# Performance work log

Hardware: AMD Instinct MI355X
Metric: run time of the kernel (lower is better)

Reference implementation:

```python
import jax, jax.numpy as jnp
import numpy as np

EMBED_DIM = 1024
NUM_HEADS = 16
HEAD_DIM = EMBED_DIM // NUM_HEADS


def setup_inputs() -> dict:
    key = jax.random.key(0)
    k_x, k_qkv, k_proj, k_pb = jax.random.split(key, 4)
    B, N = 8, 1024
    s = 1.0 / np.sqrt(EMBED_DIM)
    return {
        "x": jax.random.normal(k_x, (B, N, EMBED_DIM), dtype=jnp.float32),
        # qkv: Linear(embed_dim -> 3*all_head_dim), bias=False
        "w_qkv": jax.random.uniform(k_qkv, (EMBED_DIM, 3 * EMBED_DIM), dtype=jnp.float32, minval=-s, maxval=s),
        # proj: Linear(all_head_dim -> embed_dim), with bias
        "w_proj": jax.random.uniform(k_proj, (EMBED_DIM, EMBED_DIM), dtype=jnp.float32, minval=-s, maxval=s),
        "b_proj": jax.random.uniform(k_pb, (EMBED_DIM,), dtype=jnp.float32, minval=-s, maxval=s),
    }


def reference(x, w_qkv, w_proj, b_proj):
    B, N, _ = x.shape
    scale = HEAD_DIM ** -0.5
    qkv = jnp.einsum("bnd,de->bne", x, w_qkv)  # [B, N, 3*D]
    q, k, v = jnp.split(qkv, 3, axis=-1)
    # reshape to heads: [B, H, N, hd]
    def heads(t):
        return t.reshape(B, N, NUM_HEADS, HEAD_DIM).transpose(0, 2, 1, 3)
    q, k, v = heads(q), heads(k), heads(v)
    attn = jnp.einsum("bhqd,bhkd->bhqk", q, k) * scale
    attn = jax.nn.softmax(attn, axis=-1)
    out = jnp.einsum("bhqk,bhkd->bhqd", attn, v)
    out = out.transpose(0, 2, 1, 3).reshape(B, N, NUM_HEADS * HEAD_DIM)
    return jnp.einsum("bnd,de->bne", out, w_proj) + b_proj
```

## Files before the change

kernel.cpp:

```cpp
#include <hip/hip_runtime.h>
#include <hip/hip_bf16.h>
#include <stdint.h>

typedef __hip_bfloat16 bf16;
typedef __attribute__((ext_vector_type(8))) __bf16 bf16x8;
typedef __attribute__((ext_vector_type(4))) float f32x4;

__device__ __forceinline__ bf16x8 load8bf(const bf16* p) {
    return __builtin_bit_cast(bf16x8, *(const int4*)p);
}

__device__ __forceinline__ void async16(const bf16* g, bf16* l) {
    __builtin_amdgcn_global_load_lds((const __attribute__((address_space(1))) void*)g,
                                     (__attribute__((address_space(3))) void*)l, 16, 0, 0);
}

__global__ __launch_bounds__(256) void cast_x_kernel(const float* __restrict__ in,
                                                     bf16* __restrict__ out, int n4) {
    int i = blockIdx.x * 256 + threadIdx.x;
    if (i >= n4) return;
    float4 v = ((const float4*)in)[i];
    ushort4 o;
    o.x = __builtin_bit_cast(unsigned short, __float2bfloat16(v.x));
    o.y = __builtin_bit_cast(unsigned short, __float2bfloat16(v.y));
    o.z = __builtin_bit_cast(unsigned short, __float2bfloat16(v.z));
    o.w = __builtin_bit_cast(unsigned short, __float2bfloat16(v.w));
    ((ushort4*)out)[i] = o;
}

__global__ __launch_bounds__(256) void transpose_cast(const float* __restrict__ in,
                                                      bf16* __restrict__ out, int R, int C) {
    __shared__ float t[32][33];
    int c0 = blockIdx.x * 32, r0 = blockIdx.y * 32;
    int tx = threadIdx.x, ty = threadIdx.y;
#pragma unroll
    for (int j = 0; j < 32; j += 8)
        t[ty + j][tx] = in[(size_t)(r0 + ty + j) * C + c0 + tx];
    __syncthreads();
#pragma unroll
    for (int j = 0; j < 32; j += 8)
        out[(size_t)(c0 + ty + j) * R + r0 + tx] = __float2bfloat16(t[tx][ty + j]);
}

template <int MODE>
__global__ __launch_bounds__(256) void gemm_bt(
    const bf16* __restrict__ A, const bf16* __restrict__ Bt,
    int M, int N, int K,
    bf16* __restrict__ qo, bf16* __restrict__ ko, bf16* __restrict__ vto,
    float* __restrict__ out, const float* __restrict__ bias) {
    __shared__ __align__(16) bf16 Al0[128 * 64];
    __shared__ __align__(16) bf16 Bl0[128 * 64];
    __shared__ __align__(16) bf16 Al1[128 * 64];
    __shared__ __align__(16) bf16 Bl1[128 * 64];
    const int tid = threadIdx.x;
    const int l = tid & 63, wid = tid >> 6;
    const int lo = l & 15, hi = l >> 4;
    const int wm = wid >> 1, wn = wid & 1;
    const int m0 = blockIdx.x * 128, n0 = blockIdx.y * 128;
    const int sr = tid >> 3;
    const int cl = (tid & 7) * 8;
    const int csw = ((tid & 7) ^ (sr & 7)) * 8;

    f32x4 acc[4][4];
#pragma unroll
    for (int i = 0; i < 4; ++i)
#pragma unroll
        for (int j = 0; j < 4; ++j) acc[i][j] = f32x4{0.f, 0.f, 0.f, 0.f};

#define STAGE_A(DST, KT)                                                              \
    _Pragma("unroll") for (int s_ = 0; s_ < 4; ++s_) {                                \
        int r_ = s_ * 32 + sr;                                                        \
        async16(A + (size_t)(m0 + r_) * K + (KT) * 64 + csw, DST + r_ * 64 + cl);     \
    }
#define STAGE_B(DST, KT)                                                              \
    _Pragma("unroll") for (int s_ = 0; s_ < 4; ++s_) {                                \
        int r_ = s_ * 32 + sr;                                                        \
        async16(Bt + (size_t)(n0 + r_) * K + (KT) * 64 + csw, DST + r_ * 64 + cl);    \
    }
#define KBODY(AL, BL, ANXT, BNXT, KT, STG)                                            \
    {                                                                                 \
        __syncthreads();        \
        if (STG) { STAGE_A(ANXT, (KT) + 1); }                                         \
        __builtin_amdgcn_sched_barrier(0);                                            \
        bf16x8 af[4][2], bfv0[2][2];                                                  \
        _Pragma("unroll") for (int mt = 0; mt < 4; ++mt) {                            \
            int ar = wm * 64 + mt * 16 + lo;                                          \
            _Pragma("unroll") for (int ks = 0; ks < 2; ++ks)                          \
                af[mt][ks] = load8bf(AL + ar * 64 + ((ks * 32 + hi * 8) ^ ((ar & 7) * 8))); \
        }                                                                             \
        _Pragma("unroll") for (int nt = 0; nt < 2; ++nt) {                            \
            int br = wn * 64 + nt * 16 + lo;                                          \
            _Pragma("unroll") for (int ks = 0; ks < 2; ++ks)                          \
                bfv0[nt][ks] = load8bf(BL + br * 64 + ((ks * 32 + hi * 8) ^ ((br & 7) * 8))); \
        }                                                                             \
        _Pragma("unroll") for (int mt = 0; mt < 4; ++mt)                              \
            _Pragma("unroll") for (int nt = 0; nt < 2; ++nt)                          \
                _Pragma("unroll") for (int ks = 0; ks < 2; ++ks)                      \
                    acc[mt][nt] = __builtin_amdgcn_mfma_f32_16x16x32_bf16(            \
                        af[mt][ks], bfv0[nt][ks], acc[mt][nt], 0, 0, 0);              \
        if (STG) { STAGE_B(BNXT, (KT) + 1); }                                         \
        __builtin_amdgcn_sched_barrier(0);                                            \
        bf16x8 bfv1[2][2];                                                            \
        _Pragma("unroll") for (int nt = 0; nt < 2; ++nt) {                            \
            int br = wn * 64 + (nt + 2) * 16 + lo;                                    \
            _Pragma("unroll") for (int ks = 0; ks < 2; ++ks)                          \
                bfv1[nt][ks] = load8bf(BL + br * 64 + ((ks * 32 + hi * 8) ^ ((br & 7) * 8))); \
        }                                                                             \
        _Pragma("unroll") for (int mt = 0; mt < 4; ++mt)                              \
            _Pragma("unroll") for (int nt = 0; nt < 2; ++nt)                          \
                _Pragma("unroll") for (int ks = 0; ks < 2; ++ks)                      \
                    acc[mt][nt + 2] = __builtin_amdgcn_mfma_f32_16x16x32_bf16(        \
                        af[mt][ks], bfv1[nt][ks], acc[mt][nt + 2], 0, 0, 0);          \
    }

    const int nkt = K / 64;
    STAGE_A(Al0, 0)
    STAGE_B(Bl0, 0)
    for (int kt = 0; kt < nkt; kt += 2) {
        KBODY(Al0, Bl0, Al1, Bl1, kt, true)
        KBODY(Al1, Bl1, Al0, Bl0, kt + 1, (kt + 2 < nkt))
    }
#undef KBODY
#undef STAGE_B
#undef STAGE_A

#pragma unroll
    for (int mt = 0; mt < 4; ++mt)
#pragma unroll
        for (int nt = 0; nt < 4; ++nt)
#pragma unroll
            for (int r = 0; r < 4; ++r) {
                int row = m0 + wm * 64 + mt * 16 + hi * 4 + r;
                int col = n0 + wn * 64 + nt * 16 + lo;
                float v = acc[mt][nt][r];
                if (MODE == 0) {
                    if (col < 1024) {
                        qo[(size_t)row * 1024 + col] = __float2bfloat16(v * 0.125f);
                    } else if (col < 2048) {
                        ko[(size_t)row * 1024 + (col - 1024)] = __float2bfloat16(v);
                    } else {
                        int c = col - 2048;
                        vto[((size_t)(row >> 10) * 1024 + c) * 1024 + (row & 1023)] = __float2bfloat16(v);
                    }
                } else {
                    out[(size_t)row * N + col] = v + bias[col];
                }
            }
}

__global__ __launch_bounds__(256, 4) void flash_attn(
    const bf16* __restrict__ q,
    const bf16* __restrict__ kin,
    const bf16* __restrict__ vt,
    bf16* __restrict__ out)
{
    __shared__ __align__(16) bf16 Kl[64 * 72];
    __shared__ __align__(16) bf16 Vl[64 * 72];
    __shared__ __align__(16) bf16 Pl[4 * 32 * 72];
    const int tid = threadIdx.x;
    const int l = tid & 63, w = tid >> 6;
    const int lo = l & 15, hi = l >> 4;
    const int bid = (blockIdx.x & 7) * 128 + (blockIdx.x >> 3);
    const int qt = bid & 7, h = (bid >> 3) & 15, b = bid >> 7;
    const int sr = tid >> 3;
    const int sc = (tid & 7) * 8;

    const bf16* kbase = kin + (size_t)(b * 1024) * 1024 + h * 64;
    const bf16* vbase = vt + (size_t)(b * 1024 + h * 64) * 1024;

    bf16x8 qf[2][2];
#pragma unroll
    for (int mt = 0; mt < 2; ++mt)
#pragma unroll
        for (int ks = 0; ks < 2; ++ks) {
            int tok = qt * 128 + w * 32 + mt * 16 + lo;
            qf[mt][ks] = load8bf(q + (size_t)(b * 1024 + tok) * 1024 + h * 64 + ks * 32 + hi * 8);
        }

    float lsum[2][4];
    f32x4 oacc[2][4];
#pragma unroll
    for (int mt = 0; mt < 2; ++mt)
#pragma unroll
        for (int r = 0; r < 4; ++r) lsum[mt][r] = 0.f;
#pragma unroll
    for (int mt = 0; mt < 2; ++mt)
#pragma unroll
        for (int nt = 0; nt < 4; ++nt) oacc[mt][nt] = f32x4{0.f, 0.f, 0.f, 0.f};

    int4 kreg[2], vreg[2];
#pragma unroll
    for (int it = 0; it < 2; ++it) {
        int r = it * 32 + sr;
        kreg[it] = *(const int4*)(kbase + (size_t)r * 1024 + sc);
        vreg[it] = *(const int4*)(vbase + (size_t)r * 1024 + sc);
    }
#pragma unroll
    for (int it = 0; it < 2; ++it) {
        int r = it * 32 + sr;
        *(int4*)(Kl + r * 72 + sc) = kreg[it];
        *(int4*)(Vl + r * 72 + sc) = vreg[it];
    }
    __syncthreads();

    for (int kt = 0; kt < 16; ++kt) {
        if (kt < 15) {
#pragma unroll
            for (int it = 0; it < 2; ++it) {
                int r = it * 32 + sr;
                kreg[it] = *(const int4*)(kbase + (size_t)((kt + 1) * 64 + r) * 1024 + sc);
                vreg[it] = *(const int4*)(vbase + (size_t)r * 1024 + (kt + 1) * 64 + sc);
            }
        }

        f32x4 s[2][4];
#pragma unroll
        for (int mt = 0; mt < 2; ++mt)
#pragma unroll
            for (int nt = 0; nt < 4; ++nt) s[mt][nt] = f32x4{0.f, 0.f, 0.f, 0.f};
#pragma unroll
        for (int ks = 0; ks < 2; ++ks) {
            bf16x8 kf[4];
#pragma unroll
            for (int nt = 0; nt < 4; ++nt)
                kf[nt] = load8bf(Kl + (nt * 16 + lo) * 72 + ks * 32 + hi * 8);
#pragma unroll
            for (int mt = 0; mt < 2; ++mt)
#pragma unroll
                for (int nt = 0; nt < 4; ++nt)
                    s[mt][nt] = __builtin_amdgcn_mfma_f32_16x16x32_bf16(qf[mt][ks], kf[nt], s[mt][nt], 0, 0, 0);
        }

#pragma unroll
        for (int mt = 0; mt < 2; ++mt)
#pragma unroll
            for (int nt = 0; nt < 4; ++nt)
#pragma unroll
                for (int r = 0; r < 4; ++r) {
                    float p = __expf(s[mt][nt][r]);
                    lsum[mt][r] += p;
                    Pl[(w * 32 + mt * 16 + hi * 4 + r) * 72 + nt * 16 + lo] = __float2bfloat16(p);
                }

#pragma unroll
        for (int ks = 0; ks < 2; ++ks) {
            bf16x8 vf[4], pf[2];
#pragma unroll
            for (int nt = 0; nt < 4; ++nt)
                vf[nt] = load8bf(Vl + (nt * 16 + lo) * 72 + ks * 32 + hi * 8);
#pragma unroll
            for (int mt = 0; mt < 2; ++mt)
                pf[mt] = load8bf(Pl + (w * 32 + mt * 16 + lo) * 72 + ks * 32 + hi * 8);
#pragma unroll
            for (int mt = 0; mt < 2; ++mt)
#pragma unroll
                for (int nt = 0; nt < 4; ++nt)
                    oacc[mt][nt] = __builtin_amdgcn_mfma_f32_16x16x32_bf16(pf[mt], vf[nt], oacc[mt][nt], 0, 0, 0);
        }
        __syncthreads();

        if (kt < 15) {
#pragma unroll
            for (int it = 0; it < 2; ++it) {
                int r = it * 32 + sr;
                *(int4*)(Kl + r * 72 + sc) = kreg[it];
                *(int4*)(Vl + r * 72 + sc) = vreg[it];
            }
            __syncthreads();
        }
    }

#pragma unroll
    for (int mt = 0; mt < 2; ++mt)
#pragma unroll
        for (int r = 0; r < 4; ++r) {
#pragma unroll
            for (int off = 1; off < 16; off <<= 1)
                lsum[mt][r] += __shfl_xor(lsum[mt][r], off);
        }

#pragma unroll
    for (int mt = 0; mt < 2; ++mt)
#pragma unroll
        for (int nt = 0; nt < 4; ++nt)
#pragma unroll
            for (int r = 0; r < 4; ++r) {
                int tok = qt * 128 + w * 32 + mt * 16 + hi * 4 + r;
                int d = nt * 16 + lo;
                out[(size_t)(b * 1024 + tok) * 1024 + h * 64 + d] =
                    __float2bfloat16(oacc[mt][nt][r] / lsum[mt][r]);
            }
}

extern "C" void kernel_launch(void* const* d_in, const int* in_sizes, int n_in,
                              void* d_out, int out_size, void* d_ws, size_t ws_size,
                              hipStream_t stream) {
    const float* x      = (const float*)d_in[0];
    const float* w_qkv  = (const float*)d_in[1];
    const float* w_proj = (const float*)d_in[2];
    const float* b_proj = (const float*)d_in[3];
    float* out = (float*)d_out;

    char* ws = (char*)d_ws;
    bf16* xb     = (bf16*)(ws);
    bf16* wqkvT  = (bf16*)(ws + (16ull << 20));
    bf16* wprojT = (bf16*)(ws + (22ull << 20));
    bf16* qb     = (bf16*)(ws + (24ull << 20));
    bf16* kb     = (bf16*)(ws + (40ull << 20));
    bf16* vtb    = (bf16*)(ws + (56ull << 20));
    bf16* attn   = xb;

    cast_x_kernel<<<8192, 256, 0, stream>>>(x, xb, 2 * 1024 * 1024);
    transpose_cast<<<dim3(96, 32), dim3(32, 8), 0, stream>>>(w_qkv, wqkvT, 1024, 3072);
    transpose_cast<<<dim3(32, 32), dim3(32, 8), 0, stream>>>(w_proj, wprojT, 1024, 1024);
    gemm_bt<0><<<dim3(64, 24), 256, 0, stream>>>(xb, wqkvT, 8192, 3072, 1024,
                                                 qb, kb, vtb, nullptr, nullptr);
    flash_attn<<<1024, 256, 0, stream>>>(qb, kb, vtb, attn);
    gemm_bt<1><<<dim3(64, 8), 256, 0, stream>>>(attn, wprojT, 8192, 1024, 1024,
                                                nullptr, nullptr, nullptr, out, b_proj);
}
```

Baseline: 186.6 us.

## Double-buffer K/V tiles with async global-to-LDS loads and XOR swizzle

Replaces the register-staged K/V prefetch in the flash attention kernel with direct global_load_lds async copies into two ping-pong LDS buffers. The loop is unrolled by two so each iteration issues the next tile's copy before computing on the current one, which drops one barrier per tile. The padded 72-wide LDS rows become 64-wide rows with an XOR swizzle to avoid bank conflicts. The extra buffers raise LDS use, so the launch-bounds occupancy hint falls from 4 to 3 blocks, which may reduce latency hiding.

```diff
diff --git a/kernel.cpp b/kernel.cpp
--- a/kernel.cpp
+++ b/kernel.cpp
@@ -148,25 +148,39 @@
             }
 }
 
-__global__ __launch_bounds__(256, 4) void flash_attn(
+__global__ __launch_bounds__(256, 3) void flash_attn(
     const bf16* __restrict__ q,
     const bf16* __restrict__ kin,
     const bf16* __restrict__ vt,
     bf16* __restrict__ out)
 {
-    __shared__ __align__(16) bf16 Kl[64 * 72];
-    __shared__ __align__(16) bf16 Vl[64 * 72];
+    __shared__ __align__(16) bf16 Kl0[64 * 64];
+    __shared__ __align__(16) bf16 Vl0[64 * 64];
+    __shared__ __align__(16) bf16 Kl1[64 * 64];
+    __shared__ __align__(16) bf16 Vl1[64 * 64];
     __shared__ __align__(16) bf16 Pl[4 * 32 * 72];
     const int tid = threadIdx.x;
     const int l = tid & 63, w = tid >> 6;
     const int lo = l & 15, hi = l >> 4;
     const int bid = (blockIdx.x & 7) * 128 + (blockIdx.x >> 3);
     const int qt = bid & 7, h = (bid >> 3) & 15, b = bid >> 7;
-    const int sr = tid >> 3;
-    const int sc = (tid & 7) * 8;
+    const int ts_r = tid >> 3;
+    const int ts_c = tid & 7;
+    const int ts_csw = (ts_c ^ (ts_r & 7)) * 8;
+    const int ts_lds = tid * 8;
 
     const bf16* kbase = kin + (size_t)(b * 1024) * 1024 + h * 64;
     const bf16* vbase = vt + (size_t)(b * 1024 + h * 64) * 1024;
+
+#define STAGE_KV(KD, VD, KT)                                                          \
+    {                                                                                 \
+        async16(kbase + (size_t)((KT) * 64 + ts_r) * 1024 + ts_csw, (KD) + ts_lds);   \
+        async16(kbase + (size_t)((KT) * 64 + 32 + ts_r) * 1024 + ts_csw,              \
+                (KD) + 2048 + ts_lds);                                                \
+        async16(vbase + (size_t)ts_r * 1024 + (KT) * 64 + ts_csw, (VD) + ts_lds);     \
+        async16(vbase + (size_t)(32 + ts_r) * 1024 + (KT) * 64 + ts_csw,              \
+                (VD) + 2048 + ts_lds);                                                \
+    }
 
     bf16x8 qf[2][2];
 #pragma unroll
@@ -188,87 +202,58 @@
 #pragma unroll
         for (int nt = 0; nt < 4; ++nt) oacc[mt][nt] = f32x4{0.f, 0.f, 0.f, 0.f};
 
-    int4 kreg[2], vreg[2];
-#pragma unroll
-    for (int it = 0; it < 2; ++it) {
-        int r = it * 32 + sr;
-        kreg[it] = *(const int4*)(kbase + (size_t)r * 1024 + sc);
-        vreg[it] = *(const int4*)(vbase + (size_t)r * 1024 + sc);
-    }
-#pragma unroll
-    for (int it = 0; it < 2; ++it) {
-        int r = it * 32 + sr;
-        *(int4*)(Kl + r * 72 + sc) = kreg[it];
-        *(int4*)(Vl + r * 72 + sc) = vreg[it];
-    }
+    STAGE_KV(Kl0, Vl0, 0)
     __syncthreads();
 
-    for (int kt = 0; kt < 16; ++kt) {
-        if (kt < 15) {
-#pragma unroll
-            for (int it = 0; it < 2; ++it) {
-                int r = it * 32 + sr;
-                kreg[it] = *(const int4*)(kbase + (size_t)((kt + 1) * 64 + r) * 1024 + sc);
-                vreg[it] = *(const int4*)(vbase + (size_t)r * 1024 + (kt + 1) * 64 + sc);
-            }
-        }
-
-        f32x4 s[2][4];
-#pragma unroll
-        for (int mt = 0; mt < 2; ++mt)
-#pragma unroll
-            for (int nt = 0; nt < 4; ++nt) s[mt][nt] = f32x4{0.f, 0.f, 0.f, 0.f};
-#pragma unroll
-        for (int ks = 0; ks < 2; ++ks) {
-            bf16x8 kf[4];
-#pragma unroll
-            for (int nt = 0; nt < 4; ++nt)
-                kf[nt] = load8bf(Kl + (nt * 16 + lo) * 72 + ks * 32 + hi * 8);
-#pragma unroll
-            for (int mt = 0; mt < 2; ++mt)
-#pragma unroll
-                for (int nt = 0; nt < 4; ++nt)
-                    s[mt][nt] = __builtin_amdgcn_mfma_f32_16x16x32_bf16(qf[mt][ks], kf[nt], s[mt][nt], 0, 0, 0);
-        }
-
-#pragma unroll
-        for (int mt = 0; mt < 2; ++mt)
-#pragma unroll
-            for (int nt = 0; nt < 4; ++nt)
-#pragma unroll
-                for (int r = 0; r < 4; ++r) {
-                    float p = __expf(s[mt][nt][r]);
-                    lsum[mt][r] += p;
-                    Pl[(w * 32 + mt * 16 + hi * 4 + r) * 72 + nt * 16 + lo] = __float2bfloat16(p);
-                }
-
-#pragma unroll
-        for (int ks = 0; ks < 2; ++ks) {
-            bf16x8 vf[4], pf[2];
-#pragma unroll
-            for (int nt = 0; nt < 4; ++nt)
-                vf[nt] = load8bf(Vl + (nt * 16 + lo) * 72 + ks * 32 + hi * 8);
-#pragma unroll
-            for (int mt = 0; mt < 2; ++mt)
-                pf[mt] = load8bf(Pl + (w * 32 + mt * 16 + lo) * 72 + ks * 32 + hi * 8);
-#pragma unroll
-            for (int mt = 0; mt < 2; ++mt)
-#pragma unroll
-                for (int nt = 0; nt < 4; ++nt)
-                    oacc[mt][nt] = __builtin_amdgcn_mfma_f32_16x16x32_bf16(pf[mt], vf[nt], oacc[mt][nt], 0, 0, 0);
-        }
-        __syncthreads();
-
-        if (kt < 15) {
-#pragma unroll
-            for (int it = 0; it < 2; ++it) {
-                int r = it * 32 + sr;
-                *(int4*)(Kl + r * 72 + sc) = kreg[it];
-                *(int4*)(Vl + r * 72 + sc) = vreg[it];
-            }
-            __syncthreads();
-        }
-    }
+#define FA_ITER(KC, VC, KN, VN, KT, STG)                                              \
+    {                                                                                 \
+        if (STG) { STAGE_KV(KN, VN, (KT) + 1) }                                       \
+        __builtin_amdgcn_sched_barrier(0);                                            \
+        f32x4 s[2][4];                                                                \
+        _Pragma("unroll") for (int mt = 0; mt < 2; ++mt)                              \
+            _Pragma("unroll") for (int nt = 0; nt < 4; ++nt)                          \
+                s[mt][nt] = f32x4{0.f, 0.f, 0.f, 0.f};                                \
+        _Pragma("unroll") for (int ks = 0; ks < 2; ++ks) {                            \
+            bf16x8 kf[4];                                                             \
+            _Pragma("unroll") for (int nt = 0; nt < 4; ++nt) {                        \
+                int kr = nt * 16 + lo;                                                \
+                kf[nt] = load8bf((KC) + kr * 64 + ((ks * 32 + hi * 8) ^ ((kr & 7) * 8))); \
+            }                                                                         \
+            _Pragma("unroll") for (int mt = 0; mt < 2; ++mt)                          \
+                _Pragma("unroll") for (int nt = 0; nt < 4; ++nt)                      \
+                    s[mt][nt] = __builtin_amdgcn_mfma_f32_16x16x32_bf16(              \
+                        qf[mt][ks], kf[nt], s[mt][nt], 0, 0, 0);                      \
+        }                                                                             \
+        _Pragma("unroll") for (int mt = 0; mt < 2; ++mt)                              \
+            _Pragma("unroll") for (int nt = 0; nt < 4; ++nt)                          \
+                _Pragma("unroll") for (int r = 0; r < 4; ++r) {                       \
+                    float p = __expf(s[mt][nt][r]);                                   \
+                    lsum[mt][r] += p;                                                 \
+                    Pl[(w * 32 + mt * 16 + hi * 4 + r) * 72 + nt * 16 + lo] =         \
+                        __float2bfloat16(p);                                          \
+                }                                                                     \
+        _Pragma("unroll") for (int ks = 0; ks < 2; ++ks) {                            \
+            bf16x8 vf[4], pf[2];                                                      \
+            _Pragma("unroll") for (int nt = 0; nt < 4; ++nt) {                        \
+                int vr = nt * 16 + lo;                                                \
+                vf[nt] = load8bf((VC) + vr * 64 + ((ks * 32 + hi * 8) ^ ((vr & 7) * 8))); \
+            }                                                                         \
+            _Pragma("unroll") for (int mt = 0; mt < 2; ++mt)                          \
+                pf[mt] = load8bf(Pl + (w * 32 + mt * 16 + lo) * 72 + ks * 32 + hi * 8); \
+            _Pragma("unroll") for (int mt = 0; mt < 2; ++mt)                          \
+                _Pragma("unroll") for (int nt = 0; nt < 4; ++nt)                      \
+                    oacc[mt][nt] = __builtin_amdgcn_mfma_f32_16x16x32_bf16(           \
+                        pf[mt], vf[nt], oacc[mt][nt], 0, 0, 0);                       \
+        }                                                                             \
+        __syncthreads();        \
+    }
+
+    for (int kt = 0; kt < 16; kt += 2) {
+        FA_ITER(Kl0, Vl0, Kl1, Vl1, kt, true)
+        FA_ITER(Kl1, Vl1, Kl0, Vl0, kt + 1, (kt + 2 < 16))
+    }
+#undef FA_ITER
+#undef STAGE_KV
 
 #pragma unroll
     for (int mt = 0; mt < 2; ++mt)
```

Measured after the change: 157.1 us. 15.8% less time.
